# Kernel optimization log

Hardware: AMD Instinct MI355X
Metric: run time of the kernel (lower is better)

## Reference

```python
import jax, jax.numpy as jnp
import numpy as np

F_IN = 128
HID = 256
OUT = 64
E = 500_000
NP_ALL = 304_096   # paper nodes: seed 4096 + hop1 100000 + hop2 200000
NP_H01 = 104_096   # paper nodes kept at layer 1 (seed + hop1)
NA_ALL = 154_096   # author nodes: 4096 + 50000 + 100000
NA_H01 = 54_096    # author nodes kept at layer 1


def setup_inputs() -> dict:
    key = jax.random.key(0)
    ks = iter(jax.random.split(key, 40))
    def nrm(shape, scale=0.05):
        return jax.random.normal(next(ks), shape, dtype=jnp.float32) * scale
    inp = {
        'x_paper': nrm((NP_ALL, F_IN), 1.0),
        'x_author': nrm((NA_ALL, F_IN), 1.0),
    }
    # per-layer, per-edge-type SAGEConv params: lin_l (W,b on aggregated msgs), lin_r (W, no bias, on dst)
    for li, fin in ((0, F_IN), (1, HID)):
        for rel in ('cites', 'writes', 'rev'):
            inp[f'l{li}_{rel}_Wl'] = nrm((fin, HID))
            inp[f'l{li}_{rel}_b'] = jnp.zeros((HID,), jnp.float32)
            inp[f'l{li}_{rel}_Wr'] = nrm((fin, HID))
    inp['lin_W'] = nrm((HID, OUT))
    inp['lin_b'] = jnp.zeros((OUT,), jnp.float32)
    # edge_index per edge type per sampled hop; hop-1 edges survive trimming at layer 1
    for name, hi in (('e_cites_h1', NP_H01), ('e_cites_h2', NP_ALL),
                     ('e_writes_h1', NA_H01), ('e_writes_h2', NA_ALL),
                     ('e_rev_h1', NA_H01), ('e_rev_h2', NA_ALL)):
        inp[name] = jax.random.randint(next(ks), (2, E), 0, hi, dtype=jnp.int32)
    return inp


def _sage(x_src, x_dst, edge, Wl, b, Wr):
    # SAGEConv: mean-aggregate neighbor features, lin_l(agg) + b + lin_r(x_dst)
    n_dst = x_dst.shape[0]
    msg = x_src[edge[0]]  # [E, F] gather
    s = jax.ops.segment_sum(msg, edge[1], num_segments=n_dst)
    cnt = jax.ops.segment_sum(jnp.ones((edge.shape[1],), x_src.dtype), edge[1], num_segments=n_dst)
    mean = s / jnp.maximum(cnt, 1.0)[:, None]  # 0 for isolated dst nodes (PyG mean)
    return mean @ Wl + b + x_dst @ Wr


def reference(x_paper, x_author,
              l0_cites_Wl, l0_cites_b, l0_cites_Wr,
              l0_writes_Wl, l0_writes_b, l0_writes_Wr,
              l0_rev_Wl, l0_rev_b, l0_rev_Wr,
              l1_cites_Wl, l1_cites_b, l1_cites_Wr,
              l1_writes_Wl, l1_writes_b, l1_writes_Wr,
              l1_rev_Wl, l1_rev_b, l1_rev_Wr,
              lin_W, lin_b,
              e_cites_h1, e_cites_h2, e_writes_h1, e_writes_h2, e_rev_h1, e_rev_h2):
    # ---- layer 0: no trimming -> all nodes, all (hop1+hop2) edges ----
    ec = jnp.concatenate([e_cites_h1, e_cites_h2], axis=1)
    ew = jnp.concatenate([e_writes_h1, e_writes_h2], axis=1)
    er = jnp.concatenate([e_rev_h1, e_rev_h2], axis=1)
    p = _sage(x_paper, x_paper, ec, l0_cites_Wl, l0_cites_b, l0_cites_Wr) \
      + _sage(x_author, x_paper, ew, l0_writes_Wl, l0_writes_b, l0_writes_Wr)
    a = _sage(x_paper, x_author, er, l0_rev_Wl, l0_rev_b, l0_rev_Wr)
    xp, xa = jax.nn.relu(p), jax.nn.relu(a)
    # ---- layer 1: trim_to_layer drops last hop nodes + hop-2 edges ----
    xp, xa = xp[:NP_H01], xa[:NA_H01]
    p = _sage(xp, xp, e_cites_h1, l1_cites_Wl, l1_cites_b, l1_cites_Wr) \
      + _sage(xa, xp, e_writes_h1, l1_writes_Wl, l1_writes_b, l1_writes_Wr)
    xp = jax.nn.relu(p)
    # final Linear on 'paper' features
    return xp @ lin_W + lin_b
```

## Files before the change

kernel.cpp:

```cpp
#include <hip/hip_runtime.h>

typedef unsigned short u16;
typedef unsigned int   u32;
typedef __bf16  bf16x8 __attribute__((ext_vector_type(8)));
typedef float   floatx4 __attribute__((ext_vector_type(4)));

#define NP_ALL 304096
#define NP_H01 104096
#define NA_ALL 154096
#define NA_H01 54096

#define SEG_C0 0
#define SEG_W0 104096
#define SEG_R0 208192
#define SEG_C1 262288
#define SEG_W1 366384
#define SCAN_N 470480
#define SCAN_NBLK 1838

__device__ __forceinline__ u16 f2bf(float f){
    u32 u = __float_as_uint(f);
    return (u16)((u + 0x7fffu + ((u>>16)&1u)) >> 16);
}
__device__ __forceinline__ float blo(u32 v){ return __uint_as_float(v<<16); }
__device__ __forceinline__ float bhi(u32 v){ return __uint_as_float(v & 0xFFFF0000u); }

__global__ void wcvt_k(u16* __restrict__ dst, const float* __restrict__ src, int n){
    int t = blockIdx.x*256 + threadIdx.x;
    if (t < n) dst[t] = f2bf(src[t]);
}
__global__ void wadd_k(u16* __restrict__ dst, const float* __restrict__ a, const float* __restrict__ b, int n){
    int t = blockIdx.x*256 + threadIdx.x;
    if (t < n) dst[t] = f2bf(a[t] + b[t]);
}
__global__ void bias_k(float* __restrict__ dst, const float* __restrict__ a, const float* __restrict__ b, int n){
    int t = blockIdx.x*256 + threadIdx.x;
    if (t < n) dst[t] = a[t] + (b ? b[t] : 0.0f);
}
__global__ void cvt2_k(u32* __restrict__ dst, const float* __restrict__ src, int n2){
    int t = blockIdx.x*256 + threadIdx.x;
    if (t >= n2) return;
    dst[t] = (u32)f2bf(src[2*t]) | ((u32)f2bf(src[2*t+1])<<16);
}
__global__ void repack_k(const u16* __restrict__ Wc, int K, int N, u16* __restrict__ Wp){
    int t = blockIdx.x*256 + threadIdx.x;
    int total = (K>>5)*(N>>4)*64;
    if (t >= total) return;
    int lane = t & 63;
    int nt = (t>>6) % (N>>4);
    int kt = (t>>6) / (N>>4);
    int n  = nt*16 + (lane & 15);
    int k0 = kt*32 + (lane>>4)*8;
    u16* dst = Wp + (size_t)t*8;
    #pragma unroll
    for (int j=0;j<8;j++) dst[j] = Wc[(size_t)(k0+j)*N + n];
}

__global__ void hist_k(const int* __restrict__ edst, int nE, int limit, int* __restrict__ deg){
    int t = blockIdx.x*256 + threadIdx.x;
    if (t >= nE) return;
    int d = edst[t];
    if (d < limit) atomicAdd(deg + d, 1);
}
__global__ void scan1_k(const int* __restrict__ deg, int* __restrict__ bsum){
    __shared__ int sm[256];
    int t = blockIdx.x*256 + threadIdx.x;
    sm[threadIdx.x] = (t < SCAN_N) ? deg[t] : 0;
    __syncthreads();
    for (int s=128; s>0; s>>=1){
        if (threadIdx.x < s) sm[threadIdx.x] += sm[threadIdx.x+s];
        __syncthreads();
    }
    if (threadIdx.x == 0) bsum[blockIdx.x] = sm[0];
}
__global__ void scan2_k(int* __restrict__ bsum, int n){
    __shared__ int sm[256];
    int chunk = (n + 255) >> 8;
    int st = threadIdx.x * chunk;
    int sum = 0;
    for (int i=0;i<chunk;i++){ int idx = st+i; if (idx < n) sum += bsum[idx]; }
    sm[threadIdx.x] = sum; __syncthreads();
    int acc = sum;
    for (int s=1; s<256; s<<=1){
        int t2 = (threadIdx.x >= s) ? sm[threadIdx.x - s] : 0;
        __syncthreads();
        acc += t2; sm[threadIdx.x] = acc;
        __syncthreads();
    }
    int excl = acc - sum;
    for (int i=0;i<chunk;i++){
        int idx = st+i;
        if (idx < n){ int v = bsum[idx]; bsum[idx] = excl; excl += v; }
    }
}
__global__ void scan3_k(const int* __restrict__ deg, const int* __restrict__ bsum,
                        int* __restrict__ rowptr, int* __restrict__ wp){
    __shared__ int sm[256];
    int t = blockIdx.x*256 + threadIdx.x;
    int v = (t < SCAN_N) ? deg[t] : 0;
    sm[threadIdx.x] = v; __syncthreads();
    int acc = v;
    for (int s=1; s<256; s<<=1){
        int t2 = (threadIdx.x >= s) ? sm[threadIdx.x - s] : 0;
        __syncthreads();
        acc += t2; sm[threadIdx.x] = acc;
        __syncthreads();
    }
    int excl = acc - v + bsum[blockIdx.x];
    if (t < SCAN_N){ rowptr[t] = excl; wp[t] = excl; }
    if (t == SCAN_N-1) rowptr[SCAN_N] = excl + v;
}
__global__ void fill_k(const int* __restrict__ esrc, const int* __restrict__ edst,
                       int nE, int limit, int* __restrict__ wp, int* __restrict__ pool){
    int t = blockIdx.x*256 + threadIdx.x;
    if (t >= nE) return;
    int d = edst[t];
    if (d >= limit) return;
    int p = atomicAdd(wp + d, 1);
    pool[p] = esrc[t];
}

template<int D>
__device__ __forceinline__ void gather_mean(
    const u16* __restrict__ src, int ld,
    const int* __restrict__ rowptr, int seg, int d,
    const int* __restrict__ pool, int lane, u16* __restrict__ outrow)
{
    int b = rowptr[seg + d], e = rowptr[seg + d + 1];
    float rc = 1.0f / (float)((e - b) > 1 ? (e - b) : 1);
    if (D == 128) {
        float a0=0,a1=0,c0=0,c1=0;
        int i = b;
        for (; i+1 < e; i += 2){
            int s0 = pool[i], s1 = pool[i+1];
            u32 v0 = *(const u32*)(src + (size_t)s0*ld + 2*lane);
            u32 v1 = *(const u32*)(src + (size_t)s1*ld + 2*lane);
            a0 += blo(v0); a1 += bhi(v0);
            c0 += blo(v1); c1 += bhi(v1);
        }
        if (i < e){
            int s0 = pool[i];
            u32 v0 = *(const u32*)(src + (size_t)s0*ld + 2*lane);
            a0 += blo(v0); a1 += bhi(v0);
        }
        u32 lo = f2bf((a0+c0)*rc), hi = f2bf((a1+c1)*rc);
        *(u32*)(outrow + 2*lane) = lo | (hi<<16);
    } else {
        float a0=0,a1=0,a2=0,a3=0,c0=0,c1=0,c2=0,c3=0;
        int i = b;
        for (; i+1 < e; i += 2){
            int s0 = pool[i], s1 = pool[i+1];
            uint2 v0 = *(const uint2*)(src + (size_t)s0*ld + 4*lane);
            uint2 v1 = *(const uint2*)(src + (size_t)s1*ld + 4*lane);
            a0 += blo(v0.x); a1 += bhi(v0.x); a2 += blo(v0.y); a3 += bhi(v0.y);
            c0 += blo(v1.x); c1 += bhi(v1.x); c2 += blo(v1.y); c3 += bhi(v1.y);
        }
        if (i < e){
            int s0 = pool[i];
            uint2 v0 = *(const uint2*)(src + (size_t)s0*ld + 4*lane);
            a0 += blo(v0.x); a1 += bhi(v0.x); a2 += blo(v0.y); a3 += bhi(v0.y);
        }
        uint2 o;
        o.x = (u32)f2bf((a0+c0)*rc) | ((u32)f2bf((a1+c1)*rc)<<16);
        o.y = (u32)f2bf((a2+c2)*rc) | ((u32)f2bf((a3+c3)*rc)<<16);
        *(uint2*)(outrow + 4*lane) = o;
    }
}

__global__ __launch_bounds__(256) void gAp_k(
    const u16* __restrict__ xpb, const u16* __restrict__ xab,
    const int* __restrict__ rowptr, const int* __restrict__ pool,
    u16* __restrict__ Ap)
{
    int gid = blockIdx.x*256 + threadIdx.x;
    int wid = gid >> 6, lane = gid & 63;
    if (wid >= NP_H01) return;
    u16* row = Ap + (size_t)wid*384;
    gather_mean<128>(xpb, 128, rowptr, SEG_C0, wid, pool, lane, row);
    gather_mean<128>(xab, 128, rowptr, SEG_W0, wid, pool, lane, row + 128);
    *(u32*)(row + 256 + 2*lane) = *(const u32*)(xpb + (size_t)wid*128 + 2*lane);
}
__global__ __launch_bounds__(256) void gAa_k(
    const u16* __restrict__ xpb, const u16* __restrict__ xab,
    const int* __restrict__ rowptr, const int* __restrict__ pool,
    u16* __restrict__ Aa)
{
    int gid = blockIdx.x*256 + threadIdx.x;
    int wid = gid >> 6, lane = gid & 63;
    if (wid >= NA_H01) return;
    u16* row = Aa + (size_t)wid*256;
    gather_mean<128>(xpb, 128, rowptr, SEG_R0, wid, pool, lane, row);
    *(u32*)(row + 128 + 2*lane) = *(const u32*)(xab + (size_t)wid*128 + 2*lane);
}
__global__ __launch_bounds__(256) void gA1_k(
    const u16* __restrict__ xp, const u16* __restrict__ xa,
    const int* __restrict__ rowptr, const int* __restrict__ pool,
    u16* __restrict__ A1)
{
    int gid = blockIdx.x*256 + threadIdx.x;
    int wid = gid >> 6, lane = gid & 63;
    if (wid >= NP_H01) return;
    u16* row = A1 + (size_t)wid*768;
    gather_mean<256>(xp, 768, rowptr, SEG_C1, wid, pool, lane, row);
    gather_mean<256>(xa, 256, rowptr, SEG_W1, wid, pool, lane, row + 256);
}

template<int WROWS, int WCOLS, int WMT, int WNT, bool RELU, bool F32OUT>
__global__ __launch_bounds__(256) void gemm2_k(
    const u16* __restrict__ A, int lda, int M, int K,
    const u16* __restrict__ Wp, int nt16, const float* __restrict__ bias,
    void* __restrict__ C_, int ldc)
{
    constexpr int BNT  = WCOLS*WNT;
    constexpr int BM   = WROWS*WMT*16;
    constexpr int NSTG = 2*BNT;
    constexpr int PERW = NSTG/4;
    __shared__ __align__(16) u16 ldsB[NSTG*512];

    int wave = threadIdx.x >> 6, lane = threadIdx.x & 63;
    int quad = lane >> 4, l15 = lane & 15;
    int wr = wave / WCOLS, wc = wave % WCOLS;
    int bm0 = blockIdx.x * BM;
    int ntb = blockIdx.y * BNT;

    floatx4 acc[WMT][WNT];
    #pragma unroll
    for (int i=0;i<WMT;i++)
        #pragma unroll
        for (int j=0;j<WNT;j++) acc[i][j] = (floatx4){0.f,0.f,0.f,0.f};

    int rowb[WMT];
    #pragma unroll
    for (int i=0;i<WMT;i++){
        int r = bm0 + (wr*WMT + i)*16 + l15;
        rowb[i] = (r < M) ? r : (M-1);
    }

    int nstages = K >> 6;
    for (int s=0; s<nstages; s++){
        int kt0 = s*2;
        if (s) __syncthreads();
        #pragma unroll
        for (int i=0;i<PERW;i++){
            int g = wave*PERW + i;
            int ktl = g / BNT, ntl = g % BNT;
            const u16* gp = Wp + ((size_t)(kt0+ktl)*nt16 + ntb + ntl)*512 + lane*8;
            u16* lp = ldsB + g*512 + lane*8;
            __builtin_amdgcn_global_load_lds(
                (const __attribute__((address_space(1))) void*)gp,
                (__attribute__((address_space(3))) void*)lp, 16, 0, 0);
        }
        __syncthreads();
        #pragma unroll
        for (int ktl=0; ktl<2; ktl++){
            int kt = kt0 + ktl;
            bf16x8 af[WMT];
            #pragma unroll
            for (int i=0;i<WMT;i++)
                af[i] = *(const bf16x8*)(A + (size_t)rowb[i]*lda + kt*32 + quad*8);
            bf16x8 bfr[WNT];
            #pragma unroll
            for (int j=0;j<WNT;j++)
                bfr[j] = *(const bf16x8*)(ldsB + ((size_t)(ktl*BNT + wc*WNT + j)*64 + lane)*8);
            #pragma unroll
            for (int i=0;i<WMT;i++)
                #pragma unroll
                for (int j=0;j<WNT;j++)
                    acc[i][j] = __builtin_amdgcn_mfma_f32_16x16x32_bf16(af[i], bfr[j], acc[i][j], 0,0,0);
        }
    }
    #pragma unroll
    for (int j=0;j<WNT;j++){
        int col = (ntb + wc*WNT + j)*16 + l15;
        float bv = bias[col];
        #pragma unroll
        for (int i=0;i<WMT;i++){
            int rbase = bm0 + (wr*WMT + i)*16 + quad*4;
            #pragma unroll
            for (int ii=0; ii<4; ii++){
                int row = rbase + ii;
                if (row < M){
                    float v = acc[i][j][ii] + bv;
                    if (RELU) v = fmaxf(v, 0.0f);
                    if (F32OUT) ((float*)C_)[(size_t)row*ldc + col] = v;
                    else        ((u16*)C_)[(size_t)row*ldc + col] = f2bf(v);
                }
            }
        }
    }
}

extern "C" void kernel_launch(void* const* d_in, const int* in_sizes, int n_in,
                              void* d_out, int out_size, void* d_ws, size_t ws_size,
                              hipStream_t stream)
{
    const float* x_paper  = (const float*)d_in[0];
    const float* x_author = (const float*)d_in[1];
    const float* w_in[22];
    for (int i=0;i<22;i++) w_in[i] = (const float*)d_in[i];
    const int* e_c1 = (const int*)d_in[22]; int nE_c1 = in_sizes[22]/2;
    const int* e_c2 = (const int*)d_in[23]; int nE_c2 = in_sizes[23]/2;
    const int* e_w1 = (const int*)d_in[24]; int nE_w1 = in_sizes[24]/2;
    const int* e_w2 = (const int*)d_in[25]; int nE_w2 = in_sizes[25]/2;
    const int* e_r1 = (const int*)d_in[26]; int nE_r1 = in_sizes[26]/2;
    const int* e_r2 = (const int*)d_in[27]; int nE_r2 = in_sizes[27]/2;
    float* out = (float*)d_out;

    size_t off = 0;
    auto take = [&](size_t nb)->void* {
        void* p = (char*)d_ws + off;
        off = (off + nb + 255) & ~(size_t)255;
        return p;
    };
    u16*   A1  = (u16*)take((size_t)NP_H01*768*2);
    u16*   xa  = (u16*)take((size_t)NA_H01*256*2);
    u16*   Ap  = (u16*)take((size_t)NP_H01*384*2);
    u16*   Aa  = (u16*)take((size_t)NA_H01*256*2);
    int*   deg    = (int*)take((size_t)SCAN_N*4);
    int*   rowptr = (int*)take((size_t)(SCAN_N+1)*4);
    int*   wp     = (int*)take((size_t)SCAN_N*4);
    int*   bsum   = (int*)take((size_t)SCAN_NBLK*4);
    int*   pool   = (int*)take((size_t)4000000*4);
    u16* Wc0p = (u16*)take((size_t)384*256*2);
    u16* Wc0a = (u16*)take((size_t)256*256*2);
    u16* Wc1  = (u16*)take((size_t)768*256*2);
    u16* Wcf  = (u16*)take((size_t)256*64*2);
    u16* Wp0p = (u16*)take((size_t)384*256*2);
    u16* Wp0a = (u16*)take((size_t)256*256*2);
    u16* Wp1  = (u16*)take((size_t)768*256*2);
    u16* Wpf  = (u16*)take((size_t)256*64*2);
    float* b0p = (float*)take(256*4);
    float* b0a = (float*)take(256*4);
    float* b1  = (float*)take(256*4);
    float* bfin= (float*)take(64*4);

    u16* xpb = A1;
    u16* xab = A1 + (size_t)NP_ALL*128;
    u16* h1  = Ap;

    auto cdiv = [](long a, long b){ return (int)((a + b - 1)/b); };
    dim3 B(256);

    hipMemsetAsync(deg, 0, (size_t)SCAN_N*4, stream);

    wcvt_k<<<cdiv(32768,256),B,0,stream>>>(Wc0p,        w_in[2], 32768);
    wcvt_k<<<cdiv(32768,256),B,0,stream>>>(Wc0p+32768,  w_in[5], 32768);
    wadd_k<<<cdiv(32768,256),B,0,stream>>>(Wc0p+65536,  w_in[4], w_in[7], 32768);
    wcvt_k<<<cdiv(32768,256),B,0,stream>>>(Wc0a,        w_in[8], 32768);
    wcvt_k<<<cdiv(32768,256),B,0,stream>>>(Wc0a+32768,  w_in[10], 32768);
    wcvt_k<<<cdiv(65536,256),B,0,stream>>>(Wc1,         w_in[11], 65536);
    wcvt_k<<<cdiv(65536,256),B,0,stream>>>(Wc1+65536,   w_in[14], 65536);
    wadd_k<<<cdiv(65536,256),B,0,stream>>>(Wc1+131072,  w_in[13], w_in[16], 65536);
    wcvt_k<<<cdiv(16384,256),B,0,stream>>>(Wcf,         w_in[20], 16384);
    bias_k<<<1,B,0,stream>>>(b0p, w_in[3],  w_in[6],  256);
    bias_k<<<1,B,0,stream>>>(b0a, w_in[9],  nullptr,  256);
    bias_k<<<1,B,0,stream>>>(b1,  w_in[12], w_in[15], 256);
    bias_k<<<1,B,0,stream>>>(bfin,w_in[21], nullptr,  64);
    repack_k<<<cdiv(12288,256),B,0,stream>>>(Wc0p, 384, 256, Wp0p);
    repack_k<<<cdiv( 8192,256),B,0,stream>>>(Wc0a, 256, 256, Wp0a);
    repack_k<<<cdiv(24576,256),B,0,stream>>>(Wc1,  768, 256, Wp1);
    repack_k<<<cdiv( 2048,256),B,0,stream>>>(Wcf,  256,  64, Wpf);
    int n2p = NP_ALL*128/2, n2a = NA_ALL*128/2;
    cvt2_k<<<cdiv(n2p,256),B,0,stream>>>((u32*)xpb, x_paper,  n2p);
    cvt2_k<<<cdiv(n2a,256),B,0,stream>>>((u32*)xab, x_author, n2a);

    hist_k<<<cdiv(nE_c1,256),B,0,stream>>>(e_c1+nE_c1, nE_c1, NP_H01, deg+SEG_C0);
    hist_k<<<cdiv(nE_c2,256),B,0,stream>>>(e_c2+nE_c2, nE_c2, NP_H01, deg+SEG_C0);
    hist_k<<<cdiv(nE_w1,256),B,0,stream>>>(e_w1+nE_w1, nE_w1, NP_H01, deg+SEG_W0);
    hist_k<<<cdiv(nE_w2,256),B,0,stream>>>(e_w2+nE_w2, nE_w2, NP_H01, deg+SEG_W0);
    hist_k<<<cdiv(nE_r1,256),B,0,stream>>>(e_r1+nE_r1, nE_r1, NA_H01, deg+SEG_R0);
    hist_k<<<cdiv(nE_r2,256),B,0,stream>>>(e_r2+nE_r2, nE_r2, NA_H01, deg+SEG_R0);
    hist_k<<<cdiv(nE_c1,256),B,0,stream>>>(e_c1+nE_c1, nE_c1, NP_H01, deg+SEG_C1);
    hist_k<<<cdiv(nE_w1,256),B,0,stream>>>(e_w1+nE_w1, nE_w1, NP_H01, deg+SEG_W1);
    scan1_k<<<SCAN_NBLK,B,0,stream>>>(deg, bsum);
    scan2_k<<<1,B,0,stream>>>(bsum, SCAN_NBLK);
    scan3_k<<<SCAN_NBLK,B,0,stream>>>(deg, bsum, rowptr, wp);
    fill_k<<<cdiv(nE_c1,256),B,0,stream>>>(e_c1, e_c1+nE_c1, nE_c1, NP_H01, wp+SEG_C0, pool);
    fill_k<<<cdiv(nE_c2,256),B,0,stream>>>(e_c2, e_c2+nE_c2, nE_c2, NP_H01, wp+SEG_C0, pool);
    fill_k<<<cdiv(nE_w1,256),B,0,stream>>>(e_w1, e_w1+nE_w1, nE_w1, NP_H01, wp+SEG_W0, pool);
    fill_k<<<cdiv(nE_w2,256),B,0,stream>>>(e_w2, e_w2+nE_w2, nE_w2, NP_H01, wp+SEG_W0, pool);
    fill_k<<<cdiv(nE_r1,256),B,0,stream>>>(e_r1, e_r1+nE_r1, nE_r1, NA_H01, wp+SEG_R0, pool);
    fill_k<<<cdiv(nE_r2,256),B,0,stream>>>(e_r2, e_r2+nE_r2, nE_r2, NA_H01, wp+SEG_R0, pool);
    fill_k<<<cdiv(nE_c1,256),B,0,stream>>>(e_c1, e_c1+nE_c1, nE_c1, NP_H01, wp+SEG_C1, pool);
    fill_k<<<cdiv(nE_w1,256),B,0,stream>>>(e_w1, e_w1+nE_w1, nE_w1, NP_H01, wp+SEG_W1, pool);

    gAp_k<<<cdiv((long)NP_H01*64,256),B,0,stream>>>(xpb, xab, rowptr, pool, Ap);
    gAa_k<<<cdiv((long)NA_H01*64,256),B,0,stream>>>(xpb, xab, rowptr, pool, Aa);

    {
        dim3 g(cdiv(NP_H01,128), 2);
        gemm2_k<2,2,4,4,true,false><<<g,B,0,stream>>>(Ap, 384, NP_H01, 384, Wp0p, 16, b0p, A1+512, 768);
    }
    {
        dim3 g(cdiv(NA_H01,128), 2);
        gemm2_k<2,2,4,4,true,false><<<g,B,0,stream>>>(Aa, 256, NA_H01, 256, Wp0a, 16, b0a, xa, 256);
    }

    gA1_k<<<cdiv((long)NP_H01*64,256),B,0,stream>>>(A1+512, xa, rowptr, pool, A1);

    {
        dim3 g(cdiv(NP_H01,128), 2);
        gemm2_k<2,2,4,4,true,false><<<g,B,0,stream>>>(A1, 768, NP_H01, 768, Wp1, 16, b1, h1, 256);
    }
    {
        dim3 g(cdiv(NP_H01,256), 1);
        gemm2_k<4,1,4,4,false,true><<<g,B,0,stream>>>(h1, 256, NP_H01, 256, Wpf, 4, bfin, out, 64);
    }
}
```

Before: 1.249 ms.

## Double-buffer weight LDS tiles and A fragments in GEMM with manual waitcnt pipelining

Replaces the GEMM kernel with a software-pipelined version that double-buffers the B tiles in LDS and prefetches the A fragments into registers for the next stage while computing the current one. Explicit s_waitcnt and sched_barrier calls control the overlap, and launch bounds request 2 blocks per CU. The goal is to hide global load latency behind MFMA work. In exchange the kernel uses twice the LDS and more registers, and it depends on a hardcoded vmcnt literal that assumes a fixed load count.

Measured after the change: 1.266 ms. Within noise of the previous version (+1.4%).

```diff
diff --git a/kernel.cpp b/kernel.cpp
--- a/kernel.cpp
+++ b/kernel.cpp
@@ -206,7 +206,7 @@
 }
 
 template<int WROWS, int WCOLS, int WMT, int WNT, bool RELU, bool F32OUT>
-__global__ __launch_bounds__(256) void gemm2_k(
+__global__ __launch_bounds__(256, 2) void gemm3_k(
     const u16* __restrict__ A, int lda, int M, int K,
     const u16* __restrict__ Wp, int nt16, const float* __restrict__ bias,
     void* __restrict__ C_, int ldc)
@@ -215,7 +215,8 @@
     constexpr int BM   = WROWS*WMT*16;
     constexpr int NSTG = 2*BNT;
     constexpr int PERW = NSTG/4;
-    __shared__ __align__(16) u16 ldsB[NSTG*512];
+    static_assert(2*WMT == 8, "vmcnt(8) literal assumes 8 A-loads per stage");
+    __shared__ __align__(16) u16 ldsB[2*NSTG*512];
 
     int wave = threadIdx.x >> 6, lane = threadIdx.x & 63;
     int quad = lane >> 4, l15 = lane & 15;
@@ -229,46 +230,85 @@
         #pragma unroll
         for (int j=0;j<WNT;j++) acc[i][j] = (floatx4){0.f,0.f,0.f,0.f};
 
-    int rowb[WMT];
+    const u16* Abase[WMT];
     #pragma unroll
     for (int i=0;i<WMT;i++){
         int r = bm0 + (wr*WMT + i)*16 + l15;
-        rowb[i] = (r < M) ? r : (M-1);
+        r = (r < M) ? r : (M-1);
+        Abase[i] = A + (size_t)r*lda + quad*8;
     }
 
     int nstages = K >> 6;
-    for (int s=0; s<nstages; s++){
-        int kt0 = s*2;
-        if (s) __syncthreads();
+
+    auto stage_issue = [&](int sn, int bufsel){
         #pragma unroll
         for (int i=0;i<PERW;i++){
             int g = wave*PERW + i;
             int ktl = g / BNT, ntl = g % BNT;
-            const u16* gp = Wp + ((size_t)(kt0+ktl)*nt16 + ntb + ntl)*512 + lane*8;
-            u16* lp = ldsB + g*512 + lane*8;
+            const u16* gp = Wp + ((size_t)(sn*2+ktl)*nt16 + ntb + ntl)*512 + lane*8;
+            u16* lp = ldsB + bufsel*(NSTG*512) + g*512 + lane*8;
             __builtin_amdgcn_global_load_lds(
                 (const __attribute__((address_space(1))) void*)gp,
                 (__attribute__((address_space(3))) void*)lp, 16, 0, 0);
         }
-        __syncthreads();
+    };
+    auto a_issue = [&](int sn, bf16x8 (&dst)[2][WMT]){
+        #pragma unroll
+        for (int ktl=0; ktl<2; ktl++)
+            #pragma unroll
+            for (int i=0;i<WMT;i++)
+                dst[ktl][i] = *(const bf16x8*)(Abase[i] + (size_t)sn*64 + ktl*32);
+    };
+    auto compute = [&](int bufsel, bf16x8 (&af)[2][WMT]){
+        const u16* lb = ldsB + bufsel*(NSTG*512);
         #pragma unroll
         for (int ktl=0; ktl<2; ktl++){
-            int kt = kt0 + ktl;
-            bf16x8 af[WMT];
-            #pragma unroll
-            for (int i=0;i<WMT;i++)
-                af[i] = *(const bf16x8*)(A + (size_t)rowb[i]*lda + kt*32 + quad*8);
             bf16x8 bfr[WNT];
             #pragma unroll
             for (int j=0;j<WNT;j++)
-                bfr[j] = *(const bf16x8*)(ldsB + ((size_t)(ktl*BNT + wc*WNT + j)*64 + lane)*8);
+                bfr[j] = *(const bf16x8*)(lb + ((size_t)(ktl*BNT + wc*WNT + j)*64 + lane)*8);
             #pragma unroll
             for (int i=0;i<WMT;i++)
                 #pragma unroll
                 for (int j=0;j<WNT;j++)
-                    acc[i][j] = __builtin_amdgcn_mfma_f32_16x16x32_bf16(af[i], bfr[j], acc[i][j], 0,0,0);
-        }
-    }
+                    acc[i][j] = __builtin_amdgcn_mfma_f32_16x16x32_bf16(af[ktl][i], bfr[j], acc[i][j], 0,0,0);
+        }
+    };
+
+    bf16x8 aA[2][WMT], aB[2][WMT];
+    stage_issue(0, 0);
+    __builtin_amdgcn_sched_barrier(0);
+    a_issue(0, aA);
+    __builtin_amdgcn_sched_barrier(0);
+
+    for (int s=0; s<nstages; s+=2){
+        asm volatile("s_waitcnt lgkmcnt(0)" ::: "memory");
+        asm volatile("s_waitcnt vmcnt(8)"  ::: "memory");
+        __builtin_amdgcn_sched_barrier(0);
+        __builtin_amdgcn_s_barrier();
+        {
+            int sn = s+1;
+            stage_issue(sn, 1);
+            __builtin_amdgcn_sched_barrier(0);
+            a_issue(sn, aB);
+            __builtin_amdgcn_sched_barrier(0);
+            compute(0, aA);
+        }
+        asm volatile("s_waitcnt lgkmcnt(0)" ::: "memory");
+        asm volatile("s_waitcnt vmcnt(8)"  ::: "memory");
+        __builtin_amdgcn_sched_barrier(0);
+        __builtin_amdgcn_s_barrier();
+        {
+            int sn = (s+2 < nstages) ? s+2 : 0;
+            stage_issue(sn, 0);
+            __builtin_amdgcn_sched_barrier(0);
+            a_issue(sn, aA);
+            __builtin_amdgcn_sched_barrier(0);
+            compute(1, aB);
+        }
+    }
+    asm volatile("s_waitcnt vmcnt(0)" ::: "memory");
+
     #pragma unroll
     for (int j=0;j<WNT;j++){
         int col = (ntb + wc*WNT + j)*16 + l15;
@@ -389,21 +429,21 @@
 
     {
         dim3 g(cdiv(NP_H01,128), 2);
-        gemm2_k<2,2,4,4,true,false><<<g,B,0,stream>>>(Ap, 384, NP_H01, 384, Wp0p, 16, b0p, A1+512, 768);
+        gemm3_k<2,2,4,4,true,false><<<g,B,0,stream>>>(Ap, 384, NP_H01, 384, Wp0p, 16, b0p, A1+512, 768);
     }
     {
         dim3 g(cdiv(NA_H01,128), 2);
-        gemm2_k<2,2,4,4,true,false><<<g,B,0,stream>>>(Aa, 256, NA_H01, 256, Wp0a, 16, b0a, xa, 256);
+        gemm3_k<2,2,4,4,true,false><<<g,B,0,stream>>>(Aa, 256, NA_H01, 256, Wp0a, 16, b0a, xa, 256);
     }
 
     gA1_k<<<cdiv((long)NP_H01*64,256),B,0,stream>>>(A1+512, xa, rowptr, pool, A1);
 
     {
         dim3 g(cdiv(NP_H01,128), 2);
-        gemm2_k<2,2,4,4,true,false><<<g,B,0,stream>>>(A1, 768, NP_H01, 768, Wp1, 16, b1, h1, 256);
+        gemm3_k<2,2,4,4,true,false><<<g,B,0,stream>>>(A1, 768, NP_H01, 768, Wp1, 16, b1, h1, 256);
     }
     {
         dim3 g(cdiv(NP_H01,256), 1);
-        gemm2_k<4,1,4,4,false,true><<<g,B,0,stream>>>(h1, 256, NP_H01, 256, Wpf, 4, bfin, out, 64);
-    }
-}
+        gemm3_k<4,1,4,4,false,true><<<g,B,0,stream>>>(h1, 256, NP_H01, 256, Wpf, 4, bfin, out, 64);
+    }
+}
```
